# Kernel optimization log

Hardware: AMD Instinct MI355X
Metric: run time of the kernel (lower is better)

The kernel has to match this reference:

```python
import jax, jax.numpy as jnp
import numpy as np

B, L, H, F, K, NBINS, T = 32, 512, 512, 512, 3, 256, 4096
EPS = 1e-8  # RMSNorm epsilon
PAD = (K - 1) // 2  # =1, matches both conv paddings in the torch module


def _conv1d(x, w, b):
    # x: [B, L, Cin], w: [K, Cin, Cout]
    return jax.lax.conv_general_dilated(
        x, w, window_strides=(1,), padding=[(PAD, PAD)],
        dimension_numbers=('NLC', 'LIO', 'NLC')) + b


def _rms(x, g):
    return g * x / (jnp.sqrt(jnp.mean(x * x, axis=-1, keepdims=True)) + EPS)


def _vpred(x, mask, w1, b1, g1, w2, b2, g2, wl, bl):
    h = _rms(jax.nn.relu(_conv1d(x, w1, b1)), g1)
    h = _rms(jax.nn.relu(_conv1d(h, w2, b2)), g2)
    out = (h @ wl + bl)[..., 0]  # [B, L]
    return jnp.where(mask, 0.0, out)


def _proj(x, w1, b1, w2, b2):
    return jax.nn.relu(jax.nn.relu(x @ w1 + b1) @ w2 + b2)


def _length_regulate(x, dur, max_len):
    # Vectorized equivalent of LengthRegulator: repeat phoneme i dur[b,i] times, pad to max_len.
    cum = jnp.cumsum(dur, axis=1)               # [B, L]
    mel_len = cum[:, -1]                        # [B]
    t = jnp.arange(max_len)                     # [T]
    idx = jax.vmap(lambda c: jnp.searchsorted(c, t, side='right'))(cum)  # [B, T]
    idx = jnp.minimum(idx, x.shape[1] - 1)
    out = jnp.take_along_axis(x, idx[:, :, None], axis=1)  # [B, T, H]
    valid = (t[None, :] < mel_len[:, None])
    return out * valid[:, :, None].astype(x.dtype), mel_len


def setup_inputs() -> dict:
    key = jax.random.key(0)
    ks = iter(jax.random.split(key, 64))
    n = lambda *s: jax.random.normal(next(ks), s, jnp.float32) * 0.05
    inp = {}
    inp['x'] = jax.random.normal(next(ks), (B, L, H), jnp.float32)
    inp['embedding'] = jax.random.normal(next(ks), (B, L, H), jnp.float32)
    inp['src_mask'] = jnp.zeros((B, L), bool)
    inp['duration_target'] = jax.random.randint(next(ks), (B, L), 0, 9, jnp.int32)
    inp['pitch_target'] = jax.random.normal(next(ks), (B, L), jnp.float32)
    inp['energy_target'] = jax.random.normal(next(ks), (B, L), jnp.float32)
    inp['max_len'] = T
    for p in ['dur', 'pit', 'eng']:
        inp[p + '_w1'] = n(K, H, F); inp[p + '_b1'] = jnp.zeros(F, jnp.float32)
        inp[p + '_g1'] = jnp.ones(F, jnp.float32)
        inp[p + '_w2'] = n(K, F, F); inp[p + '_b2'] = jnp.zeros(F, jnp.float32)
        inp[p + '_g2'] = jnp.ones(F, jnp.float32)
        inp[p + '_wl'] = n(F, 1); inp[p + '_bl'] = jnp.zeros(1, jnp.float32)
    for p in ['pp', 'ep', 'sp']:
        inp[p + '_w1'] = n(H, H); inp[p + '_b1'] = jnp.zeros(H, jnp.float32)
        inp[p + '_w2'] = n(H, H); inp[p + '_b2'] = jnp.zeros(H, jnp.float32)
    inp['pitch_bins'] = jnp.linspace(-3.0, 3.0, NBINS - 1)
    inp['energy_bins'] = jnp.linspace(-3.0, 3.0, NBINS - 1)
    inp['pitch_emb'] = n(NBINS, H)
    inp['energy_emb'] = n(NBINS, H)
    return inp


def reference(x, embedding, src_mask, duration_target, pitch_target, energy_target, max_len,
              dur_w1, dur_b1, dur_g1, dur_w2, dur_b2, dur_g2, dur_wl, dur_bl,
              pit_w1, pit_b1, pit_g1, pit_w2, pit_b2, pit_g2, pit_wl, pit_bl,
              eng_w1, eng_b1, eng_g1, eng_w2, eng_b2, eng_g2, eng_wl, eng_bl,
              pp_w1, pp_b1, pp_w2, pp_b2,
              ep_w1, ep_b1, ep_w2, ep_b2,
              sp_w1, sp_b1, sp_w2, sp_b2,
              pitch_bins, energy_bins, pitch_emb, energy_emb):
    log_dur = _vpred(x, src_mask, dur_w1, dur_b1, dur_g1, dur_w2, dur_b2, dur_g2, dur_wl, dur_bl)
    pit_pred = _vpred(x + _proj(embedding, pp_w1, pp_b1, pp_w2, pp_b2), src_mask,
                      pit_w1, pit_b1, pit_g1, pit_w2, pit_b2, pit_g2, pit_wl, pit_bl)
    pitch_embedding = pitch_emb[jnp.searchsorted(pitch_bins, pitch_target)]  # torch.bucketize right=False == side='left'
    eng_pred = _vpred(x + _proj(embedding, ep_w1, ep_b1, ep_w2, ep_b2), src_mask,
                      eng_w1, eng_b1, eng_g1, eng_w2, eng_b2, eng_g2, eng_wl, eng_bl)
    energy_embedding = energy_emb[jnp.searchsorted(energy_bins, energy_target)]
    xo = x + energy_embedding + pitch_embedding + _proj(embedding, sp_w1, sp_b1, sp_w2, sp_b2)
    out, mel_len = _length_regulate(xo, duration_target, max_len)
    return (out, pit_pred, eng_pred, log_dur, mel_len)
```

## Files before the change

kernel.cpp:

```cpp
#include <hip/hip_runtime.h>

#define Bv    32
#define Lv    512
#define Hv    512
#define Fv    512
#define Tv    4096
#define Mv    (Bv*Lv)
#define NBINSv 256

#define OUT_OFF 0
#define PIT_OFF (Bv*(size_t)Tv*Hv)
#define ENG_OFF (PIT_OFF + Mv)
#define DUR_OFF (ENG_OFF + Mv)
#define MEL_OFF (DUR_OFF + Mv)

typedef unsigned short ushort;
typedef __attribute__((ext_vector_type(8))) short   bf16x8;
typedef __attribute__((ext_vector_type(4))) float   f32x4;
typedef __attribute__((ext_vector_type(8))) unsigned short u16x8;

__device__ __forceinline__ float b2f(ushort u) {
    union { float f; unsigned u; } x; x.u = ((unsigned)u) << 16; return x.f;
}
__device__ __forceinline__ ushort f2b(float f) {
    union { float f; unsigned u; } x; x.f = f;
    unsigned r = x.u + 0x7fffu + ((x.u >> 16) & 1u);
    return (ushort)(r >> 16);
}

#define GLL16(g, l) __builtin_amdgcn_global_load_lds( \
    (const __attribute__((address_space(1))) void*)(g), \
    (__attribute__((address_space(3))) void*)(l), 16, 0, 0)

#define FENCE() asm volatile("" ::: "memory")
#define BAR() do { FENCE(); __builtin_amdgcn_s_barrier(); FENCE(); } while (0)
#define VMCNT(N) asm volatile("s_waitcnt vmcnt(" #N ")" ::: "memory")

template<int NZ> struct GArgs {
    const ushort* A[NZ];
    const ushort* W[NZ];
    const float*  bias[NZ];
    ushort*       C[NZ];
};
struct RmsArgs   { const ushort* h[3]; const float* g[3]; ushort* o[3]; };
struct RlArgs    { const ushort* h[3]; const float* g[3]; const float* wl[3]; const float* bl[3]; };
struct TransArgs { const float* src[6]; ushort* dst[6]; };
struct ConvArgs  { const float* src[2]; ushort* dst[2]; };

#define MFMA_Q(IOFF, JOFF)                                               \
    do {                                                                 \
        __builtin_amdgcn_s_setprio(1);                                   \
        _Pragma("unroll")                                                \
        for (int s_ = 0; s_ < 2; ++s_)                                   \
            _Pragma("unroll")                                            \
            for (int i_ = 0; i_ < 4; ++i_)                               \
                _Pragma("unroll")                                        \
                for (int j_ = 0; j_ < 2; ++j_)                           \
                    acc[(IOFF) + i_][(JOFF) + j_] =                      \
                        __builtin_amdgcn_mfma_f32_16x16x32_bf16(         \
                            a_f[i_][s_], b_f[(JOFF) + j_][s_],           \
                            acc[(IOFF) + i_][(JOFF) + j_], 0, 0, 0);     \
        __builtin_amdgcn_s_setprio(0);                                   \
    } while (0)

template<int NTAPS, int EPI, int NZ>
__global__ __launch_bounds__(512) void gemm256_kernel(
    GArgs<NZ> ga, const float* __restrict__ res, const float* __restrict__ pe,
    const float* __restrict__ ee, const int* __restrict__ idxp,
    const int* __restrict__ idxe, const ushort* __restrict__ zp)
{
    constexpr int KTOT = NTAPS * 512;
    constexpr int NT   = KTOT / 64;
    const int z = (NZ > 1) ? blockIdx.z : 0;
    const ushort* __restrict__ A    = ga.A[z];
    const ushort* __restrict__ Bt   = ga.W[z];
    const float*  __restrict__ bias = ga.bias[z];
    ushort*       __restrict__ C    = ga.C[z];

    __shared__ ushort As[2][256][64];
    __shared__ ushort Bs[2][256][64];

    const int tid  = threadIdx.x;
    const int n0   = blockIdx.x * 256;
    const int m0   = blockIdx.y * 256;
    const int lane = tid & 63;
    const int w    = tid >> 6;
    const int wr   = w >> 2;
    const int wc   = w & 3;
    const int lr   = lane & 15;
    const int q    = lane >> 4;

    const int srow = tid >> 3;
    const int scol = ((tid & 7) ^ (srow & 7)) << 3;

    auto stageA = [&](int buf, int h, int kt) {
        const int tap = (NTAPS == 3) ? (kt >> 3) : 0;
        const int kin = (NTAPS == 3) ? ((kt & 7) << 6) : (kt << 6);
        #pragma unroll
        for (int r = 0; r < 2; ++r) {
            const int row = h * 128 + r * 64 + srow;
            const int m   = m0 + row;
            const ushort* src;
            if (NTAPS == 3) {
                const int ls = (m & (Lv - 1)) + tap - 1;
                src = ((unsigned)ls < (unsigned)Lv)
                    ? A + (size_t)(m + tap - 1) * 512 + kin + scol
                    : zp;
            } else {
                src = A + (size_t)m * 512 + kin + scol;
            }
            GLL16(src, ((ushort*)As) + buf * 16384 + h * 8192 + r * 4096 + tid * 8);
        }
    };
    auto stageB = [&](int buf, int h, int kt) {
        #pragma unroll
        for (int r = 0; r < 2; ++r) {
            const int n = n0 + h * 128 + r * 64 + srow;
            const ushort* src = Bt + (size_t)n * KTOT + kt * 64 + scol;
            GLL16(src, ((ushort*)Bs) + buf * 16384 + h * 8192 + r * 4096 + tid * 8);
        }
    };

    const int ca0 = ((q * 16) ^ ((lr & 7) << 4)) >> 1;
    const int ca1 = (((64 + q * 16)) ^ ((lr & 7) << 4)) >> 1;
    auto readA = [&](int buf, int i8, int s) -> bf16x8 {
        const int rm = wr * 128 + i8 * 16 + lr;
        return *(const bf16x8*)(((const ushort*)As) + buf * 16384 + rm * 64 + (s ? ca1 : ca0));
    };
    auto readB = [&](int buf, int j, int s) -> bf16x8 {
        const int rn = wc * 64 + j * 16 + lr;
        return *(const bf16x8*)(((const ushort*)Bs) + buf * 16384 + rn * 64 + (s ? ca1 : ca0));
    };

    f32x4 acc[8][4];
    #pragma unroll
    for (int i = 0; i < 8; ++i)
        #pragma unroll
        for (int j = 0; j < 4; ++j) {
            f32x4 zz = {0.f, 0.f, 0.f, 0.f};
            acc[i][j] = zz;
        }
    bf16x8 a_f[4][2], b_f[4][2];

    stageA(0, 0, 0); stageA(0, 1, 0);
    stageB(0, 0, 0); stageB(0, 1, 0);
    stageA(1, 0, 1);
    stageB(1, 0, 1); stageB(1, 1, 1);
    VMCNT(6);
    BAR();

    #pragma unroll 1
    for (int t = 0; t < NT; t += 2) {
        const bool pf = (t + 2 < NT);
        #pragma unroll
        for (int i = 0; i < 4; ++i) { a_f[i][0] = readA(0, i, 0); a_f[i][1] = readA(0, i, 1); }
        #pragma unroll
        for (int j = 0; j < 2; ++j) { b_f[j][0] = readB(0, j, 0); b_f[j][1] = readB(0, j, 1); }
        stageA(1, 1, t + 1);
        BAR();
        MFMA_Q(0, 0);
        BAR();
        #pragma unroll
        for (int j = 2; j < 4; ++j) { b_f[j][0] = readB(0, j, 0); b_f[j][1] = readB(0, j, 1); }
        if (pf) stageA(0, 0, t + 2);
        BAR();
        MFMA_Q(0, 2);
        BAR();
        #pragma unroll
        for (int i = 0; i < 4; ++i) { a_f[i][0] = readA(0, 4 + i, 0); a_f[i][1] = readA(0, 4 + i, 1); }
        if (pf) stageB(0, 0, t + 2);
        BAR();
        MFMA_Q(4, 0);
        BAR();
        if (pf) { stageB(0, 1, t + 2); VMCNT(6); }
        else    { VMCNT(0); }
        BAR();
        MFMA_Q(4, 2);
        BAR();
        #pragma unroll
        for (int i = 0; i < 4; ++i) { a_f[i][0] = readA(1, i, 0); a_f[i][1] = readA(1, i, 1); }
        #pragma unroll
        for (int j = 0; j < 2; ++j) { b_f[j][0] = readB(1, j, 0); b_f[j][1] = readB(1, j, 1); }
        if (pf) stageA(0, 1, t + 2);
        BAR();
        MFMA_Q(0, 0);
        BAR();
        #pragma unroll
        for (int j = 2; j < 4; ++j) { b_f[j][0] = readB(1, j, 0); b_f[j][1] = readB(1, j, 1); }
        if (pf) stageA(1, 0, t + 3);
        BAR();
        MFMA_Q(0, 2);
        BAR();
        #pragma unroll
        for (int i = 0; i < 4; ++i) { a_f[i][0] = readA(1, 4 + i, 0); a_f[i][1] = readA(1, 4 + i, 1); }
        if (pf) stageB(1, 0, t + 3);
        BAR();
        MFMA_Q(4, 0);
        BAR();
        if (pf) stageB(1, 1, t + 3);
        VMCNT(6);
        BAR();
        MFMA_Q(4, 2);
        BAR();
    }

    #pragma unroll
    for (int i = 0; i < 8; ++i) {
        #pragma unroll
        for (int r = 0; r < 4; ++r) {
            const int m = m0 + wr * 128 + i * 16 + q * 4 + r;
            const size_t ro = (size_t)m * 512;
            int ip = 0, ie = 0;
            if (EPI == 2) { ip = idxp[m]; ie = idxe[m]; }
            #pragma unroll
            for (int j = 0; j < 4; ++j) {
                const int n = n0 + wc * 64 + j * 16 + lr;
                float v = acc[i][j][r] + bias[n];
                v = fmaxf(v, 0.f);
                if (EPI >= 1) v += res[ro + n];
                if (EPI == 2) v += pe[(size_t)ip * 512 + n] + ee[(size_t)ie * 512 + n];
                C[ro + n] = f2b(v);
            }
        }
    }
}

__global__ __launch_bounds__(256) void convert_kernel(ConvArgs ca)
{
    const float* __restrict__ X  = ca.src[blockIdx.y];
    ushort*      __restrict__ Xb = ca.dst[blockIdx.y];
    const size_t i = (size_t)blockIdx.x * 256 + threadIdx.x;
    const float4 a = ((const float4*)X)[2 * i];
    const float4 b = ((const float4*)X)[2 * i + 1];
    u16x8 o;
    o[0] = f2b(a.x); o[1] = f2b(a.y); o[2] = f2b(a.z); o[3] = f2b(a.w);
    o[4] = f2b(b.x); o[5] = f2b(b.y); o[6] = f2b(b.z); o[7] = f2b(b.w);
    *(u16x8*)(Xb + i * 8) = o;
}

__global__ __launch_bounds__(256) void transpose_kernel(TransArgs ta, int Ktot)
{
    const float* __restrict__ W  = ta.src[blockIdx.z];
    ushort*      __restrict__ Wt = ta.dst[blockIdx.z];
    __shared__ float t[32][33];
    const int k0 = blockIdx.x * 32, n0 = blockIdx.y * 32;
    const int r = threadIdx.x >> 5, c = threadIdx.x & 31;
    #pragma unroll
    for (int rr = 0; rr < 4; ++rr)
        t[r + rr * 8][c] = W[(size_t)(k0 + r + rr * 8) * 512 + n0 + c];
    __syncthreads();
    #pragma unroll
    for (int rr = 0; rr < 4; ++rr)
        Wt[(size_t)(n0 + r + rr * 8) * Ktot + k0 + c] = f2b(t[c][r + rr * 8]);
}

__global__ __launch_bounds__(128) void rms_kernel(RmsArgs ra)
{
    const int z = blockIdx.y;
    const int row = blockIdx.x;
    const int tid = threadIdx.x;
    const ushort* __restrict__ h = ra.h[z];
    const ushort4 hv = ((const ushort4*)(h + (size_t)row * 512))[tid];
    const float v0 = b2f(hv.x), v1 = b2f(hv.y), v2 = b2f(hv.z), v3 = b2f(hv.w);
    float ss = v0 * v0 + v1 * v1 + v2 * v2 + v3 * v3;
    #pragma unroll
    for (int off = 32; off; off >>= 1) ss += __shfl_down(ss, off, 64);
    __shared__ float p[2];
    if ((tid & 63) == 0) p[tid >> 6] = ss;
    __syncthreads();
    const float tot = p[0] + p[1];
    const float inv = 1.f / (sqrtf(tot * (1.f / 512.f)) + 1e-8f);
    const float4 gv = ((const float4*)ra.g[z])[tid];
    ushort4 ov;
    ov.x = f2b(gv.x * v0 * inv); ov.y = f2b(gv.y * v1 * inv);
    ov.z = f2b(gv.z * v2 * inv); ov.w = f2b(gv.w * v3 * inv);
    ((ushort4*)(ra.o[z] + (size_t)row * 512))[tid] = ov;
}

__global__ __launch_bounds__(256) void rmslin_kernel(
    RlArgs ra, const unsigned char* __restrict__ mask, float* __restrict__ predbase)
{
    const int z = blockIdx.y;
    const int wave = threadIdx.x >> 6, lane = threadIdx.x & 63;
    const int row = blockIdx.x * 4 + wave;
    const ushort* __restrict__ h = ra.h[z];
    const bf16x8 hv = *(const bf16x8*)(h + (size_t)row * 512 + lane * 8);
    const float4 g0 = *(const float4*)(ra.g[z] + lane * 8);
    const float4 g1 = *(const float4*)(ra.g[z] + lane * 8 + 4);
    const float4 w0 = *(const float4*)(ra.wl[z] + lane * 8);
    const float4 w1 = *(const float4*)(ra.wl[z] + lane * 8 + 4);
    float hf[8];
    #pragma unroll
    for (int t = 0; t < 8; ++t) hf[t] = b2f((ushort)hv[t]);
    float ss = 0.f, sgw = 0.f;
    #pragma unroll
    for (int t = 0; t < 8; ++t) ss += hf[t] * hf[t];
    sgw += hf[0]*g0.x*w0.x + hf[1]*g0.y*w0.y + hf[2]*g0.z*w0.z + hf[3]*g0.w*w0.w;
    sgw += hf[4]*g1.x*w1.x + hf[5]*g1.y*w1.y + hf[6]*g1.z*w1.z + hf[7]*g1.w*w1.w;
    #pragma unroll
    for (int off = 32; off; off >>= 1) {
        ss  += __shfl_down(ss,  off, 64);
        sgw += __shfl_down(sgw, off, 64);
    }
    if (lane == 0) {
        const float inv = 1.f / (sqrtf(ss * (1.f / 512.f)) + 1e-8f);
        predbase[(size_t)z * Mv + row] = mask[row] ? 0.f : (sgw * inv + ra.bl[z][0]);
    }
}

__global__ __launch_bounds__(256) void idx_kernel(
    const float* __restrict__ pt, const float* __restrict__ et,
    const float* __restrict__ pbins, const float* __restrict__ ebins,
    int* __restrict__ idxp, int* __restrict__ idxe)
{
    __shared__ float pb[NBINSv - 1], ebn[NBINSv - 1];
    const int tid = threadIdx.x;
    if (tid < NBINSv - 1) { pb[tid] = pbins[tid]; ebn[tid] = ebins[tid]; }
    __syncthreads();
    const int m = blockIdx.x * 256 + tid;
    const float pv = pt[m], ev = et[m];
    int lo = 0, hi = NBINSv - 1;
    while (lo < hi) { int mid = (lo + hi) >> 1; if (pb[mid] < pv) lo = mid + 1; else hi = mid; }
    idxp[m] = lo;
    lo = 0; hi = NBINSv - 1;
    while (lo < hi) { int mid = (lo + hi) >> 1; if (ebn[mid] < ev) lo = mid + 1; else hi = mid; }
    idxe[m] = lo;
}

__global__ __launch_bounds__(512) void cumsum_kernel(
    const int* __restrict__ dur, int* __restrict__ cum,
    int* __restrict__ melint, float* __restrict__ melout)
{
    __shared__ int s[Lv];
    const int b = blockIdx.x, tid = threadIdx.x;
    s[tid] = dur[b * Lv + tid];
    __syncthreads();
    for (int off = 1; off < Lv; off <<= 1) {
        int t = (tid >= off) ? s[tid - off] : 0;
        __syncthreads();
        s[tid] += t;
        __syncthreads();
    }
    cum[b * Lv + tid] = s[tid];
    if (tid == Lv - 1) { melint[b] = s[tid]; melout[b] = (float)s[tid]; }
}

__global__ __launch_bounds__(256) void tmap_kernel(
    const int* __restrict__ cum, const int* __restrict__ melint,
    int* __restrict__ tmap)
{
    const int bt = blockIdx.x * 256 + threadIdx.x;
    const int b = bt >> 12;
    const int t = bt & (Tv - 1);
    const int* c = cum + b * Lv;
    int lo = 0, hi = Lv;
    while (lo < hi) { int mid = (lo + hi) >> 1; if (c[mid] <= t) lo = mid + 1; else hi = mid; }
    tmap[bt] = (t < melint[b]) ? (b * Lv + min(lo, Lv - 1)) : -1;
}

__global__ __launch_bounds__(128) void regulate_kernel(
    const ushort* __restrict__ xo, const int* __restrict__ tmap,
    float* __restrict__ out)
{
    const int bt = blockIdx.x;
    const int src = tmap[bt];
    float4 v = make_float4(0.f, 0.f, 0.f, 0.f);
    if (src >= 0) {
        const ushort4 u = ((const ushort4*)(xo + (size_t)src * 512))[threadIdx.x];
        v.x = b2f(u.x); v.y = b2f(u.y); v.z = b2f(u.z); v.w = b2f(u.w);
    }
    ((float4*)(out + (size_t)bt * 512))[threadIdx.x] = v;
}

extern "C" void kernel_launch(void* const* d_in, const int* in_sizes, int n_in,
                              void* d_out, int out_size, void* d_ws, size_t ws_size,
                              hipStream_t stream)
{
    const float* x    = (const float*)d_in[0];
    const float* emb  = (const float*)d_in[1];
    const unsigned char* mask = (const unsigned char*)d_in[2];
    const int*   durt = (const int*)d_in[3];
    const float* pt   = (const float*)d_in[4];
    const float* et   = (const float*)d_in[5];
    const float* dw1 = (const float*)d_in[7],  *db1 = (const float*)d_in[8],
               * dg1 = (const float*)d_in[9],  *dw2 = (const float*)d_in[10],
               * db2 = (const float*)d_in[11], *dg2 = (const float*)d_in[12],
               * dwl = (const float*)d_in[13], *dbl = (const float*)d_in[14];
    const float* pw1 = (const float*)d_in[15], *pb1 = (const float*)d_in[16],
               * pg1 = (const float*)d_in[17], *pw2 = (const float*)d_in[18],
               * pb2 = (const float*)d_in[19], *pg2 = (const float*)d_in[20],
               * pwl = (const float*)d_in[21], *pbl = (const float*)d_in[22];
    const float* ew1 = (const float*)d_in[23], *eb1 = (const float*)d_in[24],
               * eg1 = (const float*)d_in[25], *ew2 = (const float*)d_in[26],
               * eb2 = (const float*)d_in[27], *eg2 = (const float*)d_in[28],
               * ewl = (const float*)d_in[29], *ebl = (const float*)d_in[30];
    const float* ppw1 = (const float*)d_in[31], *ppb1 = (const float*)d_in[32],
               * ppw2 = (const float*)d_in[33], *ppb2 = (const float*)d_in[34];
    const float* epw1 = (const float*)d_in[35], *epb1 = (const float*)d_in[36],
               * epw2 = (const float*)d_in[37], *epb2 = (const float*)d_in[38];
    const float* spw1 = (const float*)d_in[39], *spb1 = (const float*)d_in[40],
               * spw2 = (const float*)d_in[41], *spb2 = (const float*)d_in[42];
    const float* pbins = (const float*)d_in[43];
    const float* ebins = (const float*)d_in[44];
    const float* pemb  = (const float*)d_in[45];
    const float* eemb  = (const float*)d_in[46];

    float* outf = (float*)d_out;

    int*    cum    = (int*)d_ws;
    int*    melint = cum + 16384;
    int*    idxp   = melint + 64;
    int*    idxe   = idxp + 16384;
    ushort* zp     = (ushort*)(idxe + 16384);
    int*    tmap   = idxe + 16448;
    ushort* xob    = (ushort*)((float*)d_ws + 262144);

    #define OBUF(i) ((ushort*)(outf + (size_t)(i) * 4194304))
    ushort* xb  = OBUF(0);   ushort* eb  = OBUF(1);
    ushort* pA0 = OBUF(2);   ushort* pA1 = OBUF(3);  ushort* pA2 = OBUF(4);
    ushort* xp  = OBUF(5);   ushort* xe  = OBUF(6);
    ushort* c0  = OBUF(7);   ushort* c1  = OBUF(8);  ushort* c2  = OBUF(9);
    ushort* r0  = OBUF(10);  ushort* r1  = OBUF(11); ushort* r2  = OBUF(12);
    ushort* wt[12];
    {
        size_t off = 13ull * 4194304;
        for (int i = 0; i < 6; ++i)  { wt[i] = (ushort*)(outf + off); off += 393216; }
        for (int i = 6; i < 12; ++i) { wt[i] = (ushort*)(outf + off); off += 131072; }
    }

    hipMemsetAsync(zp, 0, 64, stream);

    { ConvArgs ca = {{x, emb}, {xb, eb}};
      convert_kernel<<<dim3(4096, 2), 256, 0, stream>>>(ca); }
    { TransArgs ta = {{dw1, dw2, pw1, pw2, ew1, ew2}, {wt[0], wt[1], wt[2], wt[3], wt[4], wt[5]}};
      transpose_kernel<<<dim3(48, 16, 6), 256, 0, stream>>>(ta, 1536); }
    { TransArgs ta = {{ppw1, ppw2, epw1, epw2, spw1, spw2},
                      {wt[6], wt[7], wt[8], wt[9], wt[10], wt[11]}};
      transpose_kernel<<<dim3(16, 16, 6), 256, 0, stream>>>(ta, 512); }

    idx_kernel<<<Mv / 256, 256, 0, stream>>>(pt, et, pbins, ebins, idxp, idxe);
    cumsum_kernel<<<Bv, Lv, 0, stream>>>(durt, cum, melint, outf + MEL_OFF);
    tmap_kernel<<<Bv * Tv / 256, 256, 0, stream>>>(cum, melint, tmap);

    const dim3 g3(Fv / 256, Mv / 256, 3);
    const dim3 g2(Fv / 256, Mv / 256, 2);
    const dim3 g1(Fv / 256, Mv / 256, 1);

    { GArgs<3> a = {{eb, eb, eb}, {wt[6], wt[8], wt[10]}, {ppb1, epb1, spb1}, {pA0, pA1, pA2}};
      gemm256_kernel<1, 0, 3><<<g3, 512, 0, stream>>>(a, nullptr, nullptr, nullptr,
                                                      nullptr, nullptr, zp); }
    { GArgs<2> a = {{pA0, pA1}, {wt[7], wt[9]}, {ppb2, epb2}, {xp, xe}};
      gemm256_kernel<1, 1, 2><<<g2, 512, 0, stream>>>(a, x, nullptr, nullptr,
                                                      nullptr, nullptr, zp); }
    { GArgs<1> a = {{pA2}, {wt[11]}, {spb2}, {xob}};
      gemm256_kernel<1, 2, 1><<<g1, 512, 0, stream>>>(a, x, pemb, eemb, idxp, idxe, zp); }

    { GArgs<3> a = {{xp, xe, xb}, {wt[2], wt[4], wt[0]}, {pb1, eb1, db1}, {c0, c1, c2}};
      gemm256_kernel<3, 0, 3><<<g3, 512, 0, stream>>>(a, nullptr, nullptr, nullptr,
                                                      nullptr, nullptr, zp); }
    { RmsArgs ra = {{c0, c1, c2}, {pg1, eg1, dg1}, {r0, r1, r2}};
      rms_kernel<<<dim3(Mv, 3), 128, 0, stream>>>(ra); }
    { GArgs<3> a = {{r0, r1, r2}, {wt[3], wt[5], wt[1]}, {pb2, eb2, db2}, {c0, c1, c2}};
      gemm256_kernel<3, 0, 3><<<g3, 512, 0, stream>>>(a, nullptr, nullptr, nullptr,
                                                      nullptr, nullptr, zp); }
    { RlArgs ra = {{c0, c1, c2}, {pg2, eg2, dg2}, {pwl, ewl, dwl}, {pbl, ebl, dbl}};
      rmslin_kernel<<<dim3(Mv / 4, 3), 256, 0, stream>>>(ra, mask, outf + PIT_OFF); }

    regulate_kernel<<<Bv * Tv, 128, 0, stream>>>(xob, tmap, outf + OUT_OFF);
}
```

Measured before the change: 799.2 us.

## Merge projection second-layer GEMMs into one launch and interleave warp tile mapping

The two separate second-layer projection GEMM launches (pitch/energy with a residual epilogue, and speaker with the embedding-add epilogue) become one three-way batched launch. A new EPI==3 mode picks the epilogue per z-slice. This fills the GPU better and removes one launch and its tail. The warp-to-tile mapping also changes so each warp owns interleaved 64-row and 32-column chunks spread across the two staged halves, instead of one contiguous block. That aims to cut LDS bank conflicts or balance shared-memory reads, but it risks different register and epilogue access patterns.

```diff
diff --git a/kernel.cpp b/kernel.cpp
--- a/kernel.cpp
+++ b/kernel.cpp
@@ -122,13 +122,15 @@
     };
 
     const int ca0 = ((q * 16) ^ ((lr & 7) << 4)) >> 1;
-    const int ca1 = (((64 + q * 16)) ^ ((lr & 7) << 4)) >> 1;
+    const int ca1 = ((64 + q * 16) ^ ((lr & 7) << 4)) >> 1;
     auto readA = [&](int buf, int i8, int s) -> bf16x8 {
-        const int rm = wr * 128 + i8 * 16 + lr;
+        const int rm = ((i8 < 4) ? (wr * 64 + i8 * 16)
+                                 : (128 + wr * 64 + (i8 - 4) * 16)) + lr;
         return *(const bf16x8*)(((const ushort*)As) + buf * 16384 + rm * 64 + (s ? ca1 : ca0));
     };
     auto readB = [&](int buf, int j, int s) -> bf16x8 {
-        const int rn = wc * 64 + j * 16 + lr;
+        const int rn = ((j < 2) ? (wc * 32 + j * 16)
+                                : (128 + wc * 32 + (j - 2) * 16)) + lr;
         return *(const bf16x8*)(((const ushort*)Bs) + buf * 16384 + rn * 64 + (s ? ca1 : ca0));
     };
 
@@ -204,21 +206,25 @@
         BAR();
     }
 
+    int epi = EPI;
+    if (EPI == 3) epi = (z == 2) ? 2 : 1;
     #pragma unroll
     for (int i = 0; i < 8; ++i) {
+        const int mrow = (i < 4) ? (wr * 64 + i * 16) : (128 + wr * 64 + (i - 4) * 16);
         #pragma unroll
         for (int r = 0; r < 4; ++r) {
-            const int m = m0 + wr * 128 + i * 16 + q * 4 + r;
+            const int m = m0 + mrow + q * 4 + r;
             const size_t ro = (size_t)m * 512;
             int ip = 0, ie = 0;
-            if (EPI == 2) { ip = idxp[m]; ie = idxe[m]; }
+            if (EPI >= 2 && epi == 2) { ip = idxp[m]; ie = idxe[m]; }
             #pragma unroll
             for (int j = 0; j < 4; ++j) {
-                const int n = n0 + wc * 64 + j * 16 + lr;
+                const int ncol = (j < 2) ? (wc * 32 + j * 16) : (128 + wc * 32 + (j - 2) * 16);
+                const int n = n0 + ncol + lr;
                 float v = acc[i][j][r] + bias[n];
                 v = fmaxf(v, 0.f);
-                if (EPI >= 1) v += res[ro + n];
-                if (EPI == 2) v += pe[(size_t)ip * 512 + n] + ee[(size_t)ie * 512 + n];
+                if (EPI != 0 && epi >= 1) v += res[ro + n];
+                if (EPI >= 2 && epi == 2) v += pe[(size_t)ip * 512 + n] + ee[(size_t)ie * 512 + n];
                 C[ro + n] = f2b(v);
             }
         }
@@ -443,17 +449,13 @@
     tmap_kernel<<<Bv * Tv / 256, 256, 0, stream>>>(cum, melint, tmap);
 
     const dim3 g3(Fv / 256, Mv / 256, 3);
-    const dim3 g2(Fv / 256, Mv / 256, 2);
-    const dim3 g1(Fv / 256, Mv / 256, 1);
 
     { GArgs<3> a = {{eb, eb, eb}, {wt[6], wt[8], wt[10]}, {ppb1, epb1, spb1}, {pA0, pA1, pA2}};
       gemm256_kernel<1, 0, 3><<<g3, 512, 0, stream>>>(a, nullptr, nullptr, nullptr,
                                                       nullptr, nullptr, zp); }
-    { GArgs<2> a = {{pA0, pA1}, {wt[7], wt[9]}, {ppb2, epb2}, {xp, xe}};
-      gemm256_kernel<1, 1, 2><<<g2, 512, 0, stream>>>(a, x, nullptr, nullptr,
-                                                      nullptr, nullptr, zp); }
-    { GArgs<1> a = {{pA2}, {wt[11]}, {spb2}, {xob}};
-      gemm256_kernel<1, 2, 1><<<g1, 512, 0, stream>>>(a, x, pemb, eemb, idxp, idxe, zp); }
+    { GArgs<3> a = {{pA0, pA1, pA2}, {wt[7], wt[9], wt[11]}, {ppb2, epb2, spb2}, {xp, xe, xob}};
+      gemm256_kernel<1, 3, 3><<<g3, 512, 0, stream>>>(a, x, pemb, eemb,
+                                                      idxp, idxe, zp); }
 
     { GArgs<3> a = {{xp, xe, xb}, {wt[2], wt[4], wt[0]}, {pb1, eb1, db1}, {c0, c1, c2}};
       gemm256_kernel<3, 0, 3><<<g3, 512, 0, stream>>>(a, nullptr, nullptr, nullptr,
```

Measured after the change: 893.2 us. 1.12x slower.
